# Performance work log

Measured on AMD Instinct MI355X. Metric: run time of the kernel, lower is better.

Reference implementation:

```python
import jax, jax.numpy as jnp
import numpy as np


def setup_inputs() -> dict:
    key = jax.random.key(0)
    k1, k2 = jax.random.split(key)
    B, Tc, Tq, D = 8, 2048, 1024, 1024
    similarity = jax.random.normal(k1, (B, Tc, Tq), dtype=jnp.float32)
    qencode = jax.random.normal(k2, (B, Tq, D), dtype=jnp.float32)
    return {"similarity": similarity, "qencode": qencode}


def reference(similarity, qencode):
    # softmax over query axis, then weighted sum of query encodings:
    # equivalent to softmax(similarity, -1) @ qencode, avoiding the
    # [B, Tc, Tq, D] broadcasted intermediate of the original TF code.
    attn = jax.nn.softmax(similarity, axis=-1)          # [B, Tc, Tq]
    c2q = jnp.einsum("bcq,bqd->bcd", attn, qencode)     # [B, Tc, D]
    return c2q
```

## Files before the change

kernel.cpp:

```cpp
#include <hip/hip_runtime.h>
#include <hip/hip_bf16.h>
#include <stdint.h>

#define BATCH 8
#define TC 2048
#define TQ 1024
#define DD 1024

typedef __attribute__((ext_vector_type(8))) __bf16 bf16x8;
typedef __attribute__((ext_vector_type(4))) float f32x4;
typedef __attribute__((ext_vector_type(8))) ushort ushort8v;

__device__ __forceinline__ ushort f2bf(float f) {
    uint32_t u = __float_as_uint(f);
    uint32_t r = (u + 0x7fffu + ((u >> 16) & 1u)) >> 16;
    return (ushort)r;
}

__global__ __launch_bounds__(256) void prep2(const float* __restrict__ sim,
                                             const float* __restrict__ qen,
                                             ushort* __restrict__ attn,
                                             ushort* __restrict__ qt) {
    __shared__ float tile[64][65];
    const int t = threadIdx.x;
    if (blockIdx.x < 2048) {
        const int wid = t >> 6, lane = t & 63;
        const int r0 = blockIdx.x * 8 + wid * 2;

        const float4* s0 = (const float4*)(sim + (size_t)r0 * TQ);
        const float4* s1 = (const float4*)(sim + (size_t)(r0 + 1) * TQ);

        float4 x0[4], x1[4];
        #pragma unroll
        for (int j = 0; j < 4; j++) { x0[j] = s0[lane + 64 * j]; x1[j] = s1[lane + 64 * j]; }

        float m0 = -INFINITY, m1 = -INFINITY;
        #pragma unroll
        for (int j = 0; j < 4; j++) {
            m0 = fmaxf(m0, fmaxf(fmaxf(x0[j].x, x0[j].y), fmaxf(x0[j].z, x0[j].w)));
            m1 = fmaxf(m1, fmaxf(fmaxf(x1[j].x, x1[j].y), fmaxf(x1[j].z, x1[j].w)));
        }
        #pragma unroll
        for (int o = 32; o >= 1; o >>= 1) {
            m0 = fmaxf(m0, __shfl_xor(m0, o));
            m1 = fmaxf(m1, __shfl_xor(m1, o));
        }

        const float L2E = 1.4426950408889634f;
        float sa = 0.f, sb = 0.f;
        #pragma unroll
        for (int j = 0; j < 4; j++) {
            x0[j].x = exp2f((x0[j].x - m0) * L2E);
            x0[j].y = exp2f((x0[j].y - m0) * L2E);
            x0[j].z = exp2f((x0[j].z - m0) * L2E);
            x0[j].w = exp2f((x0[j].w - m0) * L2E);
            sa += (x0[j].x + x0[j].y) + (x0[j].z + x0[j].w);
            x1[j].x = exp2f((x1[j].x - m1) * L2E);
            x1[j].y = exp2f((x1[j].y - m1) * L2E);
            x1[j].z = exp2f((x1[j].z - m1) * L2E);
            x1[j].w = exp2f((x1[j].w - m1) * L2E);
            sb += (x1[j].x + x1[j].y) + (x1[j].z + x1[j].w);
        }
        #pragma unroll
        for (int o = 32; o >= 1; o >>= 1) {
            sa += __shfl_xor(sa, o);
            sb += __shfl_xor(sb, o);
        }
        const float iva = 1.0f / sa, ivb = 1.0f / sb;

        ushort4* d0 = (ushort4*)(attn + (size_t)r0 * TQ);
        ushort4* d1 = (ushort4*)(attn + (size_t)(r0 + 1) * TQ);
        #pragma unroll
        for (int j = 0; j < 4; j++) {
            ushort4 o4;
            o4.x = f2bf(x0[j].x * iva);
            o4.y = f2bf(x0[j].y * iva);
            o4.z = f2bf(x0[j].z * iva);
            o4.w = f2bf(x0[j].w * iva);
            d0[lane + 64 * j] = o4;
            o4.x = f2bf(x1[j].x * ivb);
            o4.y = f2bf(x1[j].y * ivb);
            o4.z = f2bf(x1[j].z * ivb);
            o4.w = f2bf(x1[j].w * ivb);
            d1[lane + 64 * j] = o4;
        }
    } else {
        const int bid = blockIdx.x - 2048;
        const int b = bid >> 8;
        const int rem = bid & 255;
        const int q0 = (rem >> 4) * 64;
        const int d0 = (rem & 15) * 64;
        const int r = t >> 4;
        const int c = (t & 15) * 4;

        #pragma unroll
        for (int it = 0; it < 4; it++) {
            float4 v = *(const float4*)(qen + ((size_t)b * TQ + q0 + r + it * 16) * DD + d0 + c);
            tile[r + it * 16][c + 0] = v.x;
            tile[r + it * 16][c + 1] = v.y;
            tile[r + it * 16][c + 2] = v.z;
            tile[r + it * 16][c + 3] = v.w;
        }
        __syncthreads();

        #pragma unroll
        for (int it = 0; it < 4; it++) {
            const int d = (t >> 4) + it * 16;
            const int qq = (t & 15) * 4;
            ushort4 o4;
            o4.x = f2bf(tile[qq + 0][d]);
            o4.y = f2bf(tile[qq + 1][d]);
            o4.z = f2bf(tile[qq + 2][d]);
            o4.w = f2bf(tile[qq + 3][d]);
            *(ushort4*)(qt + ((size_t)b * DD + d0 + d) * TQ + q0 + qq) = o4;
        }
    }
}

__global__ __launch_bounds__(256, 4) void gemm_bf16(const ushort* __restrict__ A,
                                                    const ushort* __restrict__ Bt,
                                                    float* __restrict__ C) {
    __shared__ __align__(16) ushort As[128 * 64];
    __shared__ __align__(16) ushort Bs[128 * 64];

    const int flat = blockIdx.x;
    const int b = flat & 7;
    const int rem = flat >> 3;
    const int group = rem >> 5;
    const int mi_t = group * 4 + (rem & 3);
    const int ni_t = (rem >> 2) & 7;
    const int tm0 = mi_t * 128;
    const int tn0 = ni_t * 128;

    const ushort* Ab = A + (size_t)b * TC * TQ;
    const ushort* Bb = Bt + (size_t)b * DD * TQ;
    float* Cb = C + (size_t)b * TC * DD;

    const int t = threadIdx.x;
    const int w = t >> 6, lane = t & 63;
    const int quad = lane >> 4, l16 = lane & 15;
    const int wm = (w >> 1) * 64, wn = (w & 1) * 64;

    f32x4 acc[4][4];
    #pragma unroll
    for (int i = 0; i < 4; i++)
        #pragma unroll
        for (int j = 0; j < 4; j++) acc[i][j] = (f32x4){0.f, 0.f, 0.f, 0.f};

    const int srow = w * 8 + (lane >> 3);
    const int sk = ((lane & 7) ^ (lane >> 3)) * 8;

    const int rkey = l16 & 7;

    for (int kk = 0; kk < TQ; kk += 64) {
        #pragma unroll
        for (int i = 0; i < 4; i++) {
            const ushort* ga = Ab + (size_t)(tm0 + i * 32 + srow) * TQ + kk + sk;
            const ushort* gb = Bb + (size_t)(tn0 + i * 32 + srow) * TQ + kk + sk;
            char* la = (char*)As + i * 4096 + w * 1024;
            char* lb = (char*)Bs + i * 4096 + w * 1024;
            __builtin_amdgcn_global_load_lds(
                (const __attribute__((address_space(1))) void*)ga,
                (__attribute__((address_space(3))) void*)la, 16, 0, 0);
            __builtin_amdgcn_global_load_lds(
                (const __attribute__((address_space(1))) void*)gb,
                (__attribute__((address_space(3))) void*)lb, 16, 0, 0);
        }
        __syncthreads();

        #pragma unroll
        for (int s = 0; s < 2; s++) {
            const int rswz = ((s * 4 + quad) ^ rkey) * 8;
            bf16x8 af[4], bfr[4];
            #pragma unroll
            for (int mi = 0; mi < 4; mi++)
                af[mi] = *(const bf16x8*)&As[(wm + mi * 16 + l16) * 64 + rswz];
            #pragma unroll
            for (int ni = 0; ni < 4; ni++)
                bfr[ni] = *(const bf16x8*)&Bs[(wn + ni * 16 + l16) * 64 + rswz];

            #pragma unroll
            for (int mi = 0; mi < 4; mi++)
                #pragma unroll
                for (int ni = 0; ni < 4; ni++)
                    acc[mi][ni] = __builtin_amdgcn_mfma_f32_16x16x32_bf16(
                        af[mi], bfr[ni], acc[mi][ni], 0, 0, 0);
        }
        __syncthreads();
    }

    #pragma unroll
    for (int mi = 0; mi < 4; mi++) {
        const int r0 = tm0 + wm + mi * 16 + quad * 4;
        #pragma unroll
        for (int ni = 0; ni < 4; ni++) {
            const int c = tn0 + wn + ni * 16 + l16;
            f32x4 v = acc[mi][ni];
            #pragma unroll
            for (int r = 0; r < 4; r++)
                __builtin_nontemporal_store(v[r], &Cb[(size_t)(r0 + r) * DD + c]);
        }
    }
}

extern "C" void kernel_launch(void* const* d_in, const int* in_sizes, int n_in,
                              void* d_out, int out_size, void* d_ws, size_t ws_size,
                              hipStream_t stream) {
    const float* sim = (const float*)d_in[0];
    const float* qen = (const float*)d_in[1];
    float* out = (float*)d_out;

    ushort* attn = (ushort*)d_ws;
    ushort* qt = (ushort*)d_ws + (size_t)BATCH * TC * TQ;

    prep2<<<2048 + 2048, 256, 0, stream>>>(sim, qen, attn, qt);
    gemm_bf16<<<BATCH * (TC / 128) * (DD / 128), 256, 0, stream>>>(attn, qt, out);
}
```

Measured before the change: 178.0 us.

## Persistent-style prep with register prefetch, relax GEMM launch bounds, plain stores

The prep kernel now runs 4x fewer blocks. Each block processes four row-pairs (softmax) or four transpose tiles in a loop and prefetches the next chunk into registers while computing the current one. The aim is to overlap memory latency and cut block launch overhead. The GEMM's launch bounds drop from 4 to 2 blocks per CU, which allows more registers per thread, and its output stores become regular rather than nontemporal. The cost is extra register pressure in prep and possibly lower GEMM occupancy.

Result: no change. 178.3 us (+0.2%).

```diff
diff --git a/kernel.cpp b/kernel.cpp
--- a/kernel.cpp
+++ b/kernel.cpp
@@ -17,107 +17,161 @@
     return (ushort)r;
 }
 
-__global__ __launch_bounds__(256) void prep2(const float* __restrict__ sim,
+__global__ __launch_bounds__(256) void prep3(const float* __restrict__ sim,
                                              const float* __restrict__ qen,
                                              ushort* __restrict__ attn,
                                              ushort* __restrict__ qt) {
     __shared__ float tile[64][65];
     const int t = threadIdx.x;
-    if (blockIdx.x < 2048) {
+    if (blockIdx.x < 512) {
         const int wid = t >> 6, lane = t & 63;
-        const int r0 = blockIdx.x * 8 + wid * 2;
-
-        const float4* s0 = (const float4*)(sim + (size_t)r0 * TQ);
-        const float4* s1 = (const float4*)(sim + (size_t)(r0 + 1) * TQ);
-
-        float4 x0[4], x1[4];
-        #pragma unroll
-        for (int j = 0; j < 4; j++) { x0[j] = s0[lane + 64 * j]; x1[j] = s1[lane + 64 * j]; }
-
-        float m0 = -INFINITY, m1 = -INFINITY;
+        const int pair0 = blockIdx.x * 16 + wid * 4;
+        const float4* sp = (const float4*)(sim + (size_t)pair0 * 2 * TQ);
+        ushort4* dp = (ushort4*)(attn + (size_t)pair0 * 2 * TQ);
+        const float L2E = 1.4426950408889634f;
+
+        float4 x0[4], x1[4], n0[4], n1[4];
         #pragma unroll
         for (int j = 0; j < 4; j++) {
-            m0 = fmaxf(m0, fmaxf(fmaxf(x0[j].x, x0[j].y), fmaxf(x0[j].z, x0[j].w)));
-            m1 = fmaxf(m1, fmaxf(fmaxf(x1[j].x, x1[j].y), fmaxf(x1[j].z, x1[j].w)));
-        }
-        #pragma unroll
-        for (int o = 32; o >= 1; o >>= 1) {
-            m0 = fmaxf(m0, __shfl_xor(m0, o));
-            m1 = fmaxf(m1, __shfl_xor(m1, o));
-        }
-
-        const float L2E = 1.4426950408889634f;
-        float sa = 0.f, sb = 0.f;
-        #pragma unroll
-        for (int j = 0; j < 4; j++) {
-            x0[j].x = exp2f((x0[j].x - m0) * L2E);
-            x0[j].y = exp2f((x0[j].y - m0) * L2E);
-            x0[j].z = exp2f((x0[j].z - m0) * L2E);
-            x0[j].w = exp2f((x0[j].w - m0) * L2E);
-            sa += (x0[j].x + x0[j].y) + (x0[j].z + x0[j].w);
-            x1[j].x = exp2f((x1[j].x - m1) * L2E);
-            x1[j].y = exp2f((x1[j].y - m1) * L2E);
-            x1[j].z = exp2f((x1[j].z - m1) * L2E);
-            x1[j].w = exp2f((x1[j].w - m1) * L2E);
-            sb += (x1[j].x + x1[j].y) + (x1[j].z + x1[j].w);
-        }
-        #pragma unroll
-        for (int o = 32; o >= 1; o >>= 1) {
-            sa += __shfl_xor(sa, o);
-            sb += __shfl_xor(sb, o);
-        }
-        const float iva = 1.0f / sa, ivb = 1.0f / sb;
-
-        ushort4* d0 = (ushort4*)(attn + (size_t)r0 * TQ);
-        ushort4* d1 = (ushort4*)(attn + (size_t)(r0 + 1) * TQ);
-        #pragma unroll
-        for (int j = 0; j < 4; j++) {
-            ushort4 o4;
-            o4.x = f2bf(x0[j].x * iva);
-            o4.y = f2bf(x0[j].y * iva);
-            o4.z = f2bf(x0[j].z * iva);
-            o4.w = f2bf(x0[j].w * iva);
-            d0[lane + 64 * j] = o4;
-            o4.x = f2bf(x1[j].x * ivb);
-            o4.y = f2bf(x1[j].y * ivb);
-            o4.z = f2bf(x1[j].z * ivb);
-            o4.w = f2bf(x1[j].w * ivb);
-            d1[lane + 64 * j] = o4;
+            x0[j] = sp[lane + 64 * j];
+            x1[j] = sp[256 + lane + 64 * j];
+        }
+
+        #pragma unroll
+        for (int n = 0; n < 4; n++) {
+            if (n < 3) {
+                const float4* np = sp + 512;
+                #pragma unroll
+                for (int j = 0; j < 4; j++) {
+                    n0[j] = np[lane + 64 * j];
+                    n1[j] = np[256 + lane + 64 * j];
+                }
+            }
+
+            float m0 = -INFINITY, m1 = -INFINITY;
+            #pragma unroll
+            for (int j = 0; j < 4; j++) {
+                m0 = fmaxf(m0, fmaxf(fmaxf(x0[j].x, x0[j].y), fmaxf(x0[j].z, x0[j].w)));
+                m1 = fmaxf(m1, fmaxf(fmaxf(x1[j].x, x1[j].y), fmaxf(x1[j].z, x1[j].w)));
+            }
+            #pragma unroll
+            for (int o = 32; o >= 1; o >>= 1) {
+                m0 = fmaxf(m0, __shfl_xor(m0, o));
+                m1 = fmaxf(m1, __shfl_xor(m1, o));
+            }
+
+            float sa = 0.f, sb = 0.f;
+            #pragma unroll
+            for (int j = 0; j < 4; j++) {
+                x0[j].x = exp2f((x0[j].x - m0) * L2E);
+                x0[j].y = exp2f((x0[j].y - m0) * L2E);
+                x0[j].z = exp2f((x0[j].z - m0) * L2E);
+                x0[j].w = exp2f((x0[j].w - m0) * L2E);
+                sa += (x0[j].x + x0[j].y) + (x0[j].z + x0[j].w);
+                x1[j].x = exp2f((x1[j].x - m1) * L2E);
+                x1[j].y = exp2f((x1[j].y - m1) * L2E);
+                x1[j].z = exp2f((x1[j].z - m1) * L2E);
+                x1[j].w = exp2f((x1[j].w - m1) * L2E);
+                sb += (x1[j].x + x1[j].y) + (x1[j].z + x1[j].w);
+            }
+            #pragma unroll
+            for (int o = 32; o >= 1; o >>= 1) {
+                sa += __shfl_xor(sa, o);
+                sb += __shfl_xor(sb, o);
+            }
+            const float iva = 1.0f / sa, ivb = 1.0f / sb;
+
+            #pragma unroll
+            for (int j = 0; j < 4; j++) {
+                ushort4 o4;
+                o4.x = f2bf(x0[j].x * iva);
+                o4.y = f2bf(x0[j].y * iva);
+                o4.z = f2bf(x0[j].z * iva);
+                o4.w = f2bf(x0[j].w * iva);
+                dp[lane + 64 * j] = o4;
+                o4.x = f2bf(x1[j].x * ivb);
+                o4.y = f2bf(x1[j].y * ivb);
+                o4.z = f2bf(x1[j].z * ivb);
+                o4.w = f2bf(x1[j].w * ivb);
+                dp[256 + lane + 64 * j] = o4;
+            }
+
+            sp += 512;
+            dp += 512;
+            if (n < 3) {
+                #pragma unroll
+                for (int j = 0; j < 4; j++) { x0[j] = n0[j]; x1[j] = n1[j]; }
+            }
         }
     } else {
-        const int bid = blockIdx.x - 2048;
-        const int b = bid >> 8;
-        const int rem = bid & 255;
-        const int q0 = (rem >> 4) * 64;
-        const int d0 = (rem & 15) * 64;
+        const int tb = blockIdx.x - 512;
         const int r = t >> 4;
         const int c = (t & 15) * 4;
-
-        #pragma unroll
-        for (int it = 0; it < 4; it++) {
-            float4 v = *(const float4*)(qen + ((size_t)b * TQ + q0 + r + it * 16) * DD + d0 + c);
-            tile[r + it * 16][c + 0] = v.x;
-            tile[r + it * 16][c + 1] = v.y;
-            tile[r + it * 16][c + 2] = v.z;
-            tile[r + it * 16][c + 3] = v.w;
-        }
-        __syncthreads();
-
-        #pragma unroll
-        for (int it = 0; it < 4; it++) {
-            const int d = (t >> 4) + it * 16;
-            const int qq = (t & 15) * 4;
-            ushort4 o4;
-            o4.x = f2bf(tile[qq + 0][d]);
-            o4.y = f2bf(tile[qq + 1][d]);
-            o4.z = f2bf(tile[qq + 2][d]);
-            o4.w = f2bf(tile[qq + 3][d]);
-            *(ushort4*)(qt + ((size_t)b * DD + d0 + d) * TQ + q0 + qq) = o4;
+        const int dl = t >> 4;
+        const int qq = (t & 15) * 4;
+
+        float4 v[4], v2[4];
+        {
+            const int tile_i = tb * 4;
+            const int b = tile_i >> 8;
+            const int rem = tile_i & 255;
+            const int q0 = (rem >> 4) * 64;
+            const int d0 = (rem & 15) * 64;
+            #pragma unroll
+            for (int it = 0; it < 4; it++)
+                v[it] = *(const float4*)(qen + ((size_t)b * TQ + q0 + r + it * 16) * DD + d0 + c);
+        }
+
+        #pragma unroll
+        for (int n = 0; n < 4; n++) {
+            const int tile_i = tb * 4 + n;
+            const int b = tile_i >> 8;
+            const int rem = tile_i & 255;
+            const int q0 = (rem >> 4) * 64;
+            const int d0 = (rem & 15) * 64;
+
+            #pragma unroll
+            for (int it = 0; it < 4; it++) {
+                tile[r + it * 16][c + 0] = v[it].x;
+                tile[r + it * 16][c + 1] = v[it].y;
+                tile[r + it * 16][c + 2] = v[it].z;
+                tile[r + it * 16][c + 3] = v[it].w;
+            }
+
+            if (n < 3) {
+                const int tj = tile_i + 1;
+                const int b2 = tj >> 8;
+                const int rem2 = tj & 255;
+                const int q02 = (rem2 >> 4) * 64;
+                const int d02 = (rem2 & 15) * 64;
+                #pragma unroll
+                for (int it = 0; it < 4; it++)
+                    v2[it] = *(const float4*)(qen + ((size_t)b2 * TQ + q02 + r + it * 16) * DD + d02 + c);
+            }
+
+            __syncthreads();
+
+            #pragma unroll
+            for (int it = 0; it < 4; it++) {
+                const int d = dl + it * 16;
+                ushort4 o4;
+                o4.x = f2bf(tile[qq + 0][d]);
+                o4.y = f2bf(tile[qq + 1][d]);
+                o4.z = f2bf(tile[qq + 2][d]);
+                o4.w = f2bf(tile[qq + 3][d]);
+                *(ushort4*)(qt + ((size_t)b * DD + d0 + d) * TQ + q0 + qq) = o4;
+            }
+
+            if (n < 3) {
+                __syncthreads();
+                #pragma unroll
+                for (int it = 0; it < 4; it++) v[it] = v2[it];
+            }
         }
     }
 }
 
-__global__ __launch_bounds__(256, 4) void gemm_bf16(const ushort* __restrict__ A,
+__global__ __launch_bounds__(256, 2) void gemm_bf16(const ushort* __restrict__ A,
                                                     const ushort* __restrict__ Bt,
                                                     float* __restrict__ C) {
     __shared__ __align__(16) ushort As[128 * 64];
@@ -197,8 +251,7 @@
             const int c = tn0 + wn + ni * 16 + l16;
             f32x4 v = acc[mi][ni];
             #pragma unroll
-            for (int r = 0; r < 4; r++)
-                __builtin_nontemporal_store(v[r], &Cb[(size_t)(r0 + r) * DD + c]);
+            for (int r = 0; r < 4; r++) Cb[(size_t)(r0 + r) * DD + c] = v[r];
         }
     }
 }
@@ -213,6 +266,6 @@
     ushort* attn = (ushort*)d_ws;
     ushort* qt = (ushort*)d_ws + (size_t)BATCH * TC * TQ;
 
-    prep2<<<2048 + 2048, 256, 0, stream>>>(sim, qen, attn, qt);
+    prep3<<<512 + 512, 256, 0, stream>>>(sim, qen, attn, qt);
     gemm_bf16<<<BATCH * (TC / 128) * (DD / 128), 256, 0, stream>>>(attn, qt, out);
 }
```
